# Kernel tuning notes

Hardware: AMD Instinct MI355X
Metric: run time of the kernel (lower is better)

The kernel has to match this reference:

```python
import jax, jax.numpy as jnp
import numpy as np

EMBED = 512
KDIM = 512
VDIM = 512
HEADS = 8
DHEAD = EMBED // HEADS  # 64
SCALE = 1.0 / np.sqrt(DHEAD).astype(np.float32)


def setup_inputs() -> dict:
    key = jax.random.key(0)
    ks = jax.random.split(key, 11)
    B, Lq, Lk = 4, 2048, 2048
    s_in = 1.0 / np.sqrt(EMBED).astype(np.float32)
    return {
        "query": jax.random.normal(ks[0], (B, Lq, EMBED), jnp.float32),
        "key": jax.random.normal(ks[1], (B, Lk, KDIM), jnp.float32),
        "value": jax.random.normal(ks[2], (B, Lk, VDIM), jnp.float32),
        "wq": jax.random.normal(ks[3], (EMBED, KDIM), jnp.float32) * s_in,
        "bq": jnp.zeros((KDIM,), jnp.float32),
        "wk": jax.random.normal(ks[4], (KDIM, KDIM), jnp.float32) * s_in,
        "bk": jnp.zeros((KDIM,), jnp.float32),
        "wv": jax.random.normal(ks[5], (VDIM, VDIM), jnp.float32) * s_in,
        "bv": jnp.zeros((VDIM,), jnp.float32),
        "wo": jax.random.normal(ks[6], (VDIM, EMBED), jnp.float32) * s_in,
        "bo": jnp.zeros((EMBED,), jnp.float32),
    }


def _split_heads(x):
    b, l, _ = x.shape
    return x.reshape(b, l, HEADS, DHEAD).transpose(0, 2, 1, 3)  # b h l d


def reference(query, key, value, wq, bq, wk, bk, wv, bv, wo, bo):
    # Linear projections (weights stored [in, out])
    q = _split_heads(query @ wq + bq)   # b h Lq d
    k = _split_heads(key @ wk + bk)     # b h Lk d
    v = _split_heads(value @ wv + bv)   # b h Lk d
    scores = jnp.einsum('bhid,bhjd->bhij', q, k) * SCALE  # b h Lq Lk
    attn = jax.nn.softmax(scores, axis=-1)
    # dropout is identity in eval mode
    ctx = jnp.einsum('bhij,bhjd->bhid', attn, v)  # b h Lq d
    b, h, l, d = ctx.shape
    ctx = ctx.transpose(0, 2, 1, 3).reshape(b, l, h * d)  # b Lq vdim
    return ctx @ wo + bo
```

## Files before the change

kernel.cpp:

```cpp
#include <hip/hip_runtime.h>
#include <stdint.h>

typedef unsigned short u16;
typedef unsigned int u32;
typedef __attribute__((ext_vector_type(8))) short short8;
typedef __attribute__((ext_vector_type(4))) float f32x4;
typedef __attribute__((ext_vector_type(16))) float f32x16;

#define DEVI static __device__ __forceinline__

DEVI u16 f2bf(float f) {
  union { float f; u32 u; } v; v.f = f;
  u32 r = v.u + 0x7FFFu + ((v.u >> 16) & 1u);
  return (u16)(r >> 16);
}

DEVI u32 pack2bf(float lo, float hi) {
  return (u32)f2bf(lo) | ((u32)f2bf(hi) << 16);
}

DEVI u32 pack2bf_fast(float lo, float hi) {
  union { float f; u32 u; } a, b;
  a.f = lo; b.f = hi;
  return __builtin_amdgcn_perm(b.u + 0x8000u, a.u + 0x8000u, 0x07060302u);
}

DEVI void gload_lds16(const u16* g, u16* l) {
  __builtin_amdgcn_global_load_lds((const __attribute__((address_space(1))) void*)g,
                                   (__attribute__((address_space(3))) void*)l, 16, 0, 0);
}

__global__ __launch_bounds__(256) void cvt3(const float* __restrict__ s0,
                                            const float* __restrict__ s1,
                                            const float* __restrict__ s2,
                                            u16* __restrict__ d0, u16* __restrict__ d1,
                                            u16* __restrict__ d2, int n) {
  int z = blockIdx.z;
  const float* src = z == 0 ? s0 : z == 1 ? s1 : s2;
  u16* dst = z == 0 ? d0 : z == 1 ? d1 : d2;
  int i = (blockIdx.x * 256 + threadIdx.x) * 4;
  if (i >= n) return;
  float4 v = *(const float4*)(src + i);
  uint2 o;
  o.x = pack2bf(v.x, v.y);
  o.y = pack2bf(v.z, v.w);
  *(uint2*)(dst + i) = o;
}

__global__ __launch_bounds__(256) void tw4(const float* __restrict__ s0, const float* __restrict__ s1,
                                           const float* __restrict__ s2, const float* __restrict__ s3,
                                           u16* __restrict__ d0, u16* __restrict__ d1,
                                           u16* __restrict__ d2, u16* __restrict__ d3) {
  int z = blockIdx.z;
  const float* src = z == 0 ? s0 : z == 1 ? s1 : z == 2 ? s2 : s3;
  u16* dst = z == 0 ? d0 : z == 1 ? d1 : z == 2 ? d2 : d3;
  __shared__ float tile[32][33];
  int tx = threadIdx.x & 31, ty = threadIdx.x >> 5;
  int bx = blockIdx.x * 32, by = blockIdx.y * 32;
#pragma unroll
  for (int i = 0; i < 32; i += 8)
    tile[ty + i][tx] = src[(size_t)(by + ty + i) * 512 + bx + tx];
  __syncthreads();
#pragma unroll
  for (int i = 0; i < 32; i += 8)
    dst[(size_t)(bx + ty + i) * 512 + by + tx] = f2bf(tile[tx][ty + i]);
}

__global__ __launch_bounds__(256) void gemm_qkv(
    const u16* __restrict__ A0, const u16* __restrict__ A1, const u16* __restrict__ A2,
    const u16* __restrict__ W0, const u16* __restrict__ W1, const u16* __restrict__ W2,
    const float* __restrict__ b0, const float* __restrict__ b1, const float* __restrict__ b2,
    u16* __restrict__ o0, u16* __restrict__ o1, u16* __restrict__ o2, float qscale) {
  const int z = blockIdx.z;
  const u16* A = z == 0 ? A0 : z == 1 ? A1 : A2;
  const u16* WT = z == 0 ? W0 : z == 1 ? W1 : W2;
  const float* bias = z == 0 ? b0 : z == 1 ? b1 : b2;
  u16* out = z == 0 ? o0 : z == 1 ? o1 : o2;
  const float sc = z == 0 ? qscale : 1.0f;

  __shared__ __align__(16) u16 As[128 * 64];
  __shared__ __align__(16) u16 Bs[128 * 64];
  const int t = threadIdx.x;
  const int w = t >> 6, lane = t & 63, quad = lane >> 4, li = lane & 15;
  const int m0 = blockIdx.x * 128, n0 = blockIdx.y * 128;
  const int wm = (w >> 1) * 64, wn = (w & 1) * 64;

  f32x4 zv = {0.f, 0.f, 0.f, 0.f};
  f32x4 acc[4][4];
#pragma unroll
  for (int mi = 0; mi < 4; mi++)
#pragma unroll
    for (int ni = 0; ni < 4; ni++) acc[mi][ni] = zv;

  for (int it = 0; it < 8; it++) {
    const int k0 = it * 64;
#pragma unroll
    for (int i = 0; i < 4; i++) {
      int s = i * 256 + t;
      int r = s >> 3, c8 = s & 7;
      gload_lds16(A + (size_t)(m0 + r) * 512 + k0 + ((c8 ^ (r & 7)) * 8),
                  &As[(i * 256 + w * 64) * 8]);
    }
#pragma unroll
    for (int i = 0; i < 4; i++) {
      int s = i * 256 + t;
      int r = s >> 3, c8 = s & 7;
      gload_lds16(WT + (size_t)(n0 + r) * 512 + k0 + ((c8 ^ (r & 7)) * 8),
                  &Bs[(i * 256 + w * 64) * 8]);
    }
    __syncthreads();
#pragma unroll
    for (int ks = 0; ks < 2; ks++) {
      short8 af[4], bf[4];
#pragma unroll
      for (int mi = 0; mi < 4; mi++) {
        int r = wm + mi * 16 + li;
        af[mi] = *(const short8*)&As[r * 64 + (((ks * 4 + quad) ^ (r & 7)) * 8)];
      }
#pragma unroll
      for (int ni = 0; ni < 4; ni++) {
        int r = wn + ni * 16 + li;
        bf[ni] = *(const short8*)&Bs[r * 64 + (((ks * 4 + quad) ^ (r & 7)) * 8)];
      }
#pragma unroll
      for (int mi = 0; mi < 4; mi++)
#pragma unroll
        for (int ni = 0; ni < 4; ni++)
          acc[mi][ni] = __builtin_amdgcn_mfma_f32_16x16x32_bf16(af[mi], bf[ni], acc[mi][ni], 0, 0, 0);
    }
    __syncthreads();
  }

  float bv[4];
#pragma unroll
  for (int ni = 0; ni < 4; ni++) bv[ni] = bias[n0 + wn + ni * 16 + li];
#pragma unroll
  for (int mi = 0; mi < 4; mi++)
#pragma unroll
    for (int ni = 0; ni < 4; ni++)
#pragma unroll
      for (int r = 0; r < 4; r++) {
        int row = m0 + wm + mi * 16 + quad * 4 + r;
        int col = n0 + wn + ni * 16 + li;
        out[(size_t)row * 512 + col] = f2bf((acc[mi][ni][r] + bv[ni]) * sc);
      }
}

__global__ __launch_bounds__(256) void gemm_out(const u16* __restrict__ A,
                                                const u16* __restrict__ WT,
                                                const float* __restrict__ bias,
                                                float* __restrict__ out) {
  __shared__ __align__(16) u16 As[128 * 64];
  __shared__ __align__(16) u16 Bs[64 * 64];
  const int t = threadIdx.x;
  const int w = t >> 6, lane = t & 63, quad = lane >> 4, li = lane & 15;
  const int m0 = blockIdx.x * 128, n0 = blockIdx.y * 64;
  const int wm = (w >> 1) * 64, wn = (w & 1) * 32;

  f32x4 zv = {0.f, 0.f, 0.f, 0.f};
  f32x4 acc[4][2];
#pragma unroll
  for (int mi = 0; mi < 4; mi++)
#pragma unroll
    for (int ni = 0; ni < 2; ni++) acc[mi][ni] = zv;

  for (int it = 0; it < 8; it++) {
    const int k0 = it * 64;
#pragma unroll
    for (int i = 0; i < 4; i++) {
      int s = i * 256 + t;
      int r = s >> 3, c8 = s & 7;
      gload_lds16(A + (size_t)(m0 + r) * 512 + k0 + ((c8 ^ (r & 7)) * 8),
                  &As[(i * 256 + w * 64) * 8]);
    }
#pragma unroll
    for (int i = 0; i < 2; i++) {
      int s = i * 256 + t;
      int r = s >> 3, c8 = s & 7;
      gload_lds16(WT + (size_t)(n0 + r) * 512 + k0 + ((c8 ^ (r & 7)) * 8),
                  &Bs[(i * 256 + w * 64) * 8]);
    }
    __syncthreads();
#pragma unroll
    for (int ks = 0; ks < 2; ks++) {
      short8 af[4], bf[2];
#pragma unroll
      for (int mi = 0; mi < 4; mi++) {
        int r = wm + mi * 16 + li;
        af[mi] = *(const short8*)&As[r * 64 + (((ks * 4 + quad) ^ (r & 7)) * 8)];
      }
#pragma unroll
      for (int ni = 0; ni < 2; ni++) {
        int r = wn + ni * 16 + li;
        bf[ni] = *(const short8*)&Bs[r * 64 + (((ks * 4 + quad) ^ (r & 7)) * 8)];
      }
#pragma unroll
      for (int mi = 0; mi < 4; mi++)
#pragma unroll
        for (int ni = 0; ni < 2; ni++)
          acc[mi][ni] = __builtin_amdgcn_mfma_f32_16x16x32_bf16(af[mi], bf[ni], acc[mi][ni], 0, 0, 0);
    }
    __syncthreads();
  }

  float bv[2];
#pragma unroll
  for (int ni = 0; ni < 2; ni++) bv[ni] = bias[n0 + wn + ni * 16 + li];
#pragma unroll
  for (int mi = 0; mi < 4; mi++)
#pragma unroll
    for (int ni = 0; ni < 2; ni++)
#pragma unroll
      for (int r = 0; r < 4; r++) {
        int row = m0 + wm + mi * 16 + quad * 4 + r;
        int col = n0 + wn + ni * 16 + li;
        out[(size_t)row * 512 + col] = acc[mi][ni][r] + bv[ni];
      }
}

__global__ __launch_bounds__(256) void transpose_v(const u16* __restrict__ Vp,
                                                   u16* __restrict__ VT) {
  __shared__ u16 tile[64][65];
  int b = blockIdx.z, h = blockIdx.y, l0 = blockIdx.x * 64;
  int t = threadIdx.x;
#pragma unroll
  for (int p = 0; p < 2; p++) {
    int r = (t >> 3) + p * 32, c = (t & 7) * 8;
    short8 v = *(const short8*)&Vp[(size_t)(b * 2048 + l0 + r) * 512 + h * 64 + c];
#pragma unroll
    for (int i = 0; i < 8; i++) tile[r][c + i] = (u16)v[i];
  }
  __syncthreads();
  int d = t >> 2, lc = (t & 3) * 16;
  u16* o = VT + ((size_t)((b * 8 + h) * 64 + d)) * 2048 + l0 + lc;
  short8 o0, o1;
#pragma unroll
  for (int i = 0; i < 8; i++) o0[i] = (short)tile[lc + i][d];
#pragma unroll
  for (int i = 0; i < 8; i++) o1[i] = (short)tile[lc + 8 + i][d];
  *(short8*)(o) = o0;
  *(short8*)(o + 8) = o1;
}

__global__ __launch_bounds__(256) void attn(const u16* __restrict__ Qp,
                                            const u16* __restrict__ Kp,
                                            const u16* __restrict__ VT,
                                            u16* __restrict__ ctx) {
  __shared__ __align__(16) u16 Ks[64 * 64];
  __shared__ __align__(16) u16 Vs[64 * 64];
  __shared__ __align__(16) u16 Ps[4][32 * 64];
  const int t = threadIdx.x;
  const int w = t >> 6, lane = t & 63;
  const int qn = lane & 31, hi = lane >> 5;
  const int b = blockIdx.z, h = blockIdx.y;
  const int q0 = blockIdx.x * 128 + w * 32;

  short8 qf[4];
  {
    const u16* qg = Qp + (size_t)(b * 2048 + q0 + qn) * 512 + h * 64 + hi * 8;
#pragma unroll
    for (int ks = 0; ks < 4; ks++) qf[ks] = *(const short8*)(qg + ks * 16);
  }

  f32x16 o[2];
#pragma unroll
  for (int dt = 0; dt < 2; dt++)
#pragma unroll
    for (int r = 0; r < 16; r++) o[dt][r] = 0.f;
  float lsum = 0.f;

  u16* pw = &Ps[w][0];

  for (int kt = 0; kt < 32; kt++) {
    const int k0 = kt * 64;
#pragma unroll
    for (int i = 0; i < 2; i++) {
      int s = i * 256 + t;
      int r = s >> 3, c8 = s & 7;
      gload_lds16(Kp + (size_t)(b * 2048 + k0 + r) * 512 + h * 64 + ((c8 ^ (r & 7)) * 8),
                  &Ks[(i * 256 + w * 64) * 8]);
      gload_lds16(VT + ((size_t)((b * 8 + h) * 64 + r)) * 2048 + k0 + ((c8 ^ (r & 7)) * 8),
                  &Vs[(i * 256 + w * 64) * 8]);
    }
    __syncthreads();

    f32x16 st[2];
#pragma unroll
    for (int kjt = 0; kjt < 2; kjt++) {
#pragma unroll
      for (int r = 0; r < 16; r++) st[kjt][r] = 0.f;
#pragma unroll
      for (int ks = 0; ks < 4; ks++) {
        int m = kjt * 32 + qn;
        short8 ka = *(const short8*)&Ks[m * 64 + (((ks * 2 + hi) ^ (m & 7)) * 8)];
        st[kjt] = __builtin_amdgcn_mfma_f32_32x32x16_bf16(ka, qf[ks], st[kjt], 0, 0, 0);
      }
    }

#pragma unroll
    for (int kjt = 0; kjt < 2; kjt++)
#pragma unroll
      for (int k8 = 0; k8 < 4; k8++) {
        float p0 = __builtin_amdgcn_exp2f(st[kjt][k8 * 4 + 0]);
        float p1 = __builtin_amdgcn_exp2f(st[kjt][k8 * 4 + 1]);
        float p2 = __builtin_amdgcn_exp2f(st[kjt][k8 * 4 + 2]);
        float p3 = __builtin_amdgcn_exp2f(st[kjt][k8 * 4 + 3]);
        lsum += (p0 + p1) + (p2 + p3);
        uint2 dw;
        dw.x = pack2bf_fast(p0, p1);
        dw.y = pack2bf_fast(p2, p3);
        int chunk = kjt * 4 + k8;
        *(uint2*)&pw[qn * 64 + ((chunk ^ (qn & 7)) * 8) + hi * 4] = dw;
      }

    short8 pb[4];
#pragma unroll
    for (int ks = 0; ks < 4; ks++)
      pb[ks] = *(const short8*)&pw[qn * 64 + (((ks * 2 + hi) ^ (qn & 7)) * 8)];
#pragma unroll
    for (int dt = 0; dt < 2; dt++)
#pragma unroll
      for (int ks = 0; ks < 4; ks++) {
        int m = dt * 32 + qn;
        short8 va = *(const short8*)&Vs[m * 64 + (((ks * 2 + hi) ^ (m & 7)) * 8)];
        o[dt] = __builtin_amdgcn_mfma_f32_32x32x16_bf16(va, pb[ks], o[dt], 0, 0, 0);
      }
    __syncthreads();
  }

  float l = lsum + __shfl_xor(lsum, 32);
  float inv = 1.0f / l;

#pragma unroll
  for (int dt = 0; dt < 2; dt++)
#pragma unroll
    for (int k8 = 0; k8 < 4; k8++) {
      uint2 dw;
      dw.x = pack2bf_fast(o[dt][k8 * 4 + 0] * inv, o[dt][k8 * 4 + 1] * inv);
      dw.y = pack2bf_fast(o[dt][k8 * 4 + 2] * inv, o[dt][k8 * 4 + 3] * inv);
      int chunk = dt * 4 + k8;
      *(uint2*)&pw[qn * 64 + ((chunk ^ (qn & 7)) * 8) + hi * 4] = dw;
    }
  __builtin_amdgcn_s_waitcnt(0);
  int q = lane >> 1, half = lane & 1;
  u16* dst = ctx + (size_t)(b * 2048 + q0 + q) * 512 + h * 64 + half * 32;
#pragma unroll
  for (int cc = 0; cc < 4; cc++) {
    int chunk = half * 4 + cc;
    *(short8*)(dst + cc * 8) = *(const short8*)&pw[q * 64 + ((chunk ^ (q & 7)) * 8)];
  }
}

extern "C" void kernel_launch(void* const* d_in, const int* in_sizes, int n_in,
                              void* d_out, int out_size, void* d_ws, size_t ws_size,
                              hipStream_t stream) {
  const float* query = (const float*)d_in[0];
  const float* key_ = (const float*)d_in[1];
  const float* value = (const float*)d_in[2];
  const float* wq = (const float*)d_in[3];
  const float* bq = (const float*)d_in[4];
  const float* wk = (const float*)d_in[5];
  const float* bk = (const float*)d_in[6];
  const float* wv = (const float*)d_in[7];
  const float* bv = (const float*)d_in[8];
  const float* wo = (const float*)d_in[9];
  const float* bo = (const float*)d_in[10];

  char* ws = (char*)d_ws;
  const size_t SZ_X = (size_t)8192 * 512 * 2;
  const size_t SZ_W = (size_t)512 * 512 * 2;
  u16* qb = (u16*)(ws);
  u16* kb = (u16*)(ws + SZ_X);
  u16* vb = (u16*)(ws + 2 * SZ_X);
  u16* wqT = (u16*)(ws + 3 * SZ_X);
  u16* wkT = (u16*)(ws + 3 * SZ_X + SZ_W);
  u16* wvT = (u16*)(ws + 3 * SZ_X + 2 * SZ_W);
  u16* woT = (u16*)(ws + 3 * SZ_X + 3 * SZ_W);
  u16* Qp = (u16*)(ws + 3 * SZ_X + 4 * SZ_W);
  u16* Kp = (u16*)(ws + 4 * SZ_X + 4 * SZ_W);
  u16* Vp = (u16*)(ws + 5 * SZ_X + 4 * SZ_W);
  u16* VTp = kb;
  u16* ctx = qb;

  const float C1 = 0.125f * 1.44269504088896f;

  const int n = 8192 * 512;
  cvt3<<<dim3(n / 1024, 1, 3), 256, 0, stream>>>(query, key_, value, qb, kb, vb, n);
  tw4<<<dim3(16, 16, 4), 256, 0, stream>>>(wq, wk, wv, wo, wqT, wkT, wvT, woT);
  gemm_qkv<<<dim3(64, 4, 3), 256, 0, stream>>>(qb, kb, vb, wqT, wkT, wvT, bq, bk, bv,
                                               Qp, Kp, Vp, C1);
  transpose_v<<<dim3(32, 8, 4), 256, 0, stream>>>(Vp, VTp);
  attn<<<dim3(16, 8, 4), 256, 0, stream>>>(Qp, Kp, VTp, ctx);
  gemm_out<<<dim3(64, 8), 256, 0, stream>>>(ctx, woT, bo, (float*)d_out);
}
```

Before: 207.1 us.

## Fuse input conversion and V transpose into QKV GEMM, split attention over keys

Removes the separate fp32-to-bf16 conversion kernel by converting the inputs inside the QKV GEMM load path. The V-transpose kernel is also dropped: the V projection now writes its output already transposed. Attention now splits the key range in two across blocks, with 128-thread blocks each handling 128 queries. This gives a split-K partial output plus row sums, merged and normalized by a new reduce kernel. The output GEMM uses a wider N tile, and the LDS swizzle gains an extra XOR term. The cost is fp32 partial-output traffic and one extra reduction launch, in exchange for fewer launches and more attention parallelism.

```diff
diff --git a/kernel.cpp b/kernel.cpp
--- a/kernel.cpp
+++ b/kernel.cpp
@@ -30,22 +30,7 @@
                                    (__attribute__((address_space(3))) void*)l, 16, 0, 0);
 }
 
-__global__ __launch_bounds__(256) void cvt3(const float* __restrict__ s0,
-                                            const float* __restrict__ s1,
-                                            const float* __restrict__ s2,
-                                            u16* __restrict__ d0, u16* __restrict__ d1,
-                                            u16* __restrict__ d2, int n) {
-  int z = blockIdx.z;
-  const float* src = z == 0 ? s0 : z == 1 ? s1 : s2;
-  u16* dst = z == 0 ? d0 : z == 1 ? d1 : d2;
-  int i = (blockIdx.x * 256 + threadIdx.x) * 4;
-  if (i >= n) return;
-  float4 v = *(const float4*)(src + i);
-  uint2 o;
-  o.x = pack2bf(v.x, v.y);
-  o.y = pack2bf(v.z, v.w);
-  *(uint2*)(dst + i) = o;
-}
+DEVI int sw8(int chunk, int r) { return ((chunk ^ (r & 7) ^ ((r >> 3) & 3)) * 8); }
 
 __global__ __launch_bounds__(256) void tw4(const float* __restrict__ s0, const float* __restrict__ s1,
                                            const float* __restrict__ s2, const float* __restrict__ s3,
@@ -67,15 +52,14 @@
 }
 
 __global__ __launch_bounds__(256) void gemm_qkv(
-    const u16* __restrict__ A0, const u16* __restrict__ A1, const u16* __restrict__ A2,
+    const float* __restrict__ A0, const float* __restrict__ A1, const float* __restrict__ A2,
     const u16* __restrict__ W0, const u16* __restrict__ W1, const u16* __restrict__ W2,
     const float* __restrict__ b0, const float* __restrict__ b1, const float* __restrict__ b2,
-    u16* __restrict__ o0, u16* __restrict__ o1, u16* __restrict__ o2, float qscale) {
+    u16* __restrict__ oq, u16* __restrict__ ok, u16* __restrict__ vt, float qscale) {
   const int z = blockIdx.z;
-  const u16* A = z == 0 ? A0 : z == 1 ? A1 : A2;
+  const float* A = z == 0 ? A0 : z == 1 ? A1 : A2;
   const u16* WT = z == 0 ? W0 : z == 1 ? W1 : W2;
   const float* bias = z == 0 ? b0 : z == 1 ? b1 : b2;
-  u16* out = z == 0 ? o0 : z == 1 ? o1 : o2;
   const float sc = z == 0 ? qscale : 1.0f;
 
   __shared__ __align__(16) u16 As[128 * 64];
@@ -92,21 +76,27 @@
 #pragma unroll
     for (int ni = 0; ni < 4; ni++) acc[mi][ni] = zv;
 
+  const int rA = t >> 3, cA = t & 7;
   for (int it = 0; it < 8; it++) {
     const int k0 = it * 64;
 #pragma unroll
-    for (int i = 0; i < 4; i++) {
-      int s = i * 256 + t;
+    for (int p = 0; p < 4; p++) {
+      int r = p * 32 + rA;
+      const float* ga = A + (size_t)(m0 + r) * 512 + k0 + cA * 8;
+      float4 f0 = *(const float4*)ga;
+      float4 f1 = *(const float4*)(ga + 4);
+      uint4 pk;
+      pk.x = pack2bf_fast(f0.x, f0.y);
+      pk.y = pack2bf_fast(f0.z, f0.w);
+      pk.z = pack2bf_fast(f1.x, f1.y);
+      pk.w = pack2bf_fast(f1.z, f1.w);
+      *(uint4*)&As[r * 64 + sw8(cA, r)] = pk;
+    }
+#pragma unroll
+    for (int p = 0; p < 4; p++) {
+      int s = p * 256 + t;
       int r = s >> 3, c8 = s & 7;
-      gload_lds16(A + (size_t)(m0 + r) * 512 + k0 + ((c8 ^ (r & 7)) * 8),
-                  &As[(i * 256 + w * 64) * 8]);
-    }
-#pragma unroll
-    for (int i = 0; i < 4; i++) {
-      int s = i * 256 + t;
-      int r = s >> 3, c8 = s & 7;
-      gload_lds16(WT + (size_t)(n0 + r) * 512 + k0 + ((c8 ^ (r & 7)) * 8),
-                  &Bs[(i * 256 + w * 64) * 8]);
+      gload_lds16(WT + (size_t)(n0 + r) * 512 + k0 + sw8(c8, r), &Bs[(p * 256 + w * 64) * 8]);
     }
     __syncthreads();
 #pragma unroll
@@ -115,12 +105,12 @@
 #pragma unroll
       for (int mi = 0; mi < 4; mi++) {
         int r = wm + mi * 16 + li;
-        af[mi] = *(const short8*)&As[r * 64 + (((ks * 4 + quad) ^ (r & 7)) * 8)];
+        af[mi] = *(const short8*)&As[r * 64 + sw8(ks * 4 + quad, r)];
       }
 #pragma unroll
       for (int ni = 0; ni < 4; ni++) {
         int r = wn + ni * 16 + li;
-        bf[ni] = *(const short8*)&Bs[r * 64 + (((ks * 4 + quad) ^ (r & 7)) * 8)];
+        bf[ni] = *(const short8*)&Bs[r * 64 + sw8(ks * 4 + quad, r)];
       }
 #pragma unroll
       for (int mi = 0; mi < 4; mi++)
@@ -134,16 +124,34 @@
   float bv[4];
 #pragma unroll
   for (int ni = 0; ni < 4; ni++) bv[ni] = bias[n0 + wn + ni * 16 + li];
-#pragma unroll
-  for (int mi = 0; mi < 4; mi++)
-#pragma unroll
-    for (int ni = 0; ni < 4; ni++)
-#pragma unroll
-      for (int r = 0; r < 4; r++) {
-        int row = m0 + wm + mi * 16 + quad * 4 + r;
+
+  if (z < 2) {
+    u16* out = z == 0 ? oq : ok;
+#pragma unroll
+    for (int mi = 0; mi < 4; mi++)
+#pragma unroll
+      for (int ni = 0; ni < 4; ni++)
+#pragma unroll
+        for (int r = 0; r < 4; r++) {
+          int row = m0 + wm + mi * 16 + quad * 4 + r;
+          int col = n0 + wn + ni * 16 + li;
+          out[(size_t)row * 512 + col] = f2bf((acc[mi][ni][r] + bv[ni]) * sc);
+        }
+  } else {
+#pragma unroll
+    for (int mi = 0; mi < 4; mi++)
+#pragma unroll
+      for (int ni = 0; ni < 4; ni++) {
         int col = n0 + wn + ni * 16 + li;
-        out[(size_t)row * 512 + col] = f2bf((acc[mi][ni][r] + bv[ni]) * sc);
-      }
+        int h = col >> 6, dd = col & 63;
+        int row0 = m0 + wm + mi * 16 + quad * 4;
+        int bb = row0 >> 11, l0 = row0 & 2047;
+        uint2 dw;
+        dw.x = pack2bf(acc[mi][ni][0] + bv[ni], acc[mi][ni][1] + bv[ni]);
+        dw.y = pack2bf(acc[mi][ni][2] + bv[ni], acc[mi][ni][3] + bv[ni]);
+        *(uint2*)&vt[((size_t)((bb * 8 + h) * 64 + dd)) * 2048 + l0] = dw;
+      }
+  }
 }
 
 __global__ __launch_bounds__(256) void gemm_out(const u16* __restrict__ A,
@@ -151,65 +159,58 @@
                                                 const float* __restrict__ bias,
                                                 float* __restrict__ out) {
   __shared__ __align__(16) u16 As[128 * 64];
-  __shared__ __align__(16) u16 Bs[64 * 64];
+  __shared__ __align__(16) u16 Bs[128 * 64];
   const int t = threadIdx.x;
   const int w = t >> 6, lane = t & 63, quad = lane >> 4, li = lane & 15;
-  const int m0 = blockIdx.x * 128, n0 = blockIdx.y * 64;
-  const int wm = (w >> 1) * 64, wn = (w & 1) * 32;
+  const int m0 = blockIdx.x * 128, n0 = blockIdx.y * 128;
+  const int wm = (w >> 1) * 64, wn = (w & 1) * 64;
 
   f32x4 zv = {0.f, 0.f, 0.f, 0.f};
-  f32x4 acc[4][2];
+  f32x4 acc[4][4];
 #pragma unroll
   for (int mi = 0; mi < 4; mi++)
 #pragma unroll
-    for (int ni = 0; ni < 2; ni++) acc[mi][ni] = zv;
+    for (int ni = 0; ni < 4; ni++) acc[mi][ni] = zv;
 
   for (int it = 0; it < 8; it++) {
     const int k0 = it * 64;
 #pragma unroll
-    for (int i = 0; i < 4; i++) {
-      int s = i * 256 + t;
+    for (int p = 0; p < 4; p++) {
+      int s = p * 256 + t;
       int r = s >> 3, c8 = s & 7;
-      gload_lds16(A + (size_t)(m0 + r) * 512 + k0 + ((c8 ^ (r & 7)) * 8),
-                  &As[(i * 256 + w * 64) * 8]);
-    }
-#pragma unroll
-    for (int i = 0; i < 2; i++) {
-      int s = i * 256 + t;
-      int r = s >> 3, c8 = s & 7;
-      gload_lds16(WT + (size_t)(n0 + r) * 512 + k0 + ((c8 ^ (r & 7)) * 8),
-                  &Bs[(i * 256 + w * 64) * 8]);
+      gload_lds16(A + (size_t)(m0 + r) * 512 + k0 + sw8(c8, r), &As[(p * 256 + w * 64) * 8]);
+      gload_lds16(WT + (size_t)(n0 + r) * 512 + k0 + sw8(c8, r), &Bs[(p * 256 + w * 64) * 8]);
     }
     __syncthreads();
 #pragma unroll
     for (int ks = 0; ks < 2; ks++) {
-      short8 af[4], bf[2];
+      short8 af[4], bf[4];
 #pragma unroll
       for (int mi = 0; mi < 4; mi++) {
         int r = wm + mi * 16 + li;
-        af[mi] = *(const short8*)&As[r * 64 + (((ks * 4 + quad) ^ (r & 7)) * 8)];
-      }
-#pragma unroll
-      for (int ni = 0; ni < 2; ni++) {
+        af[mi] = *(const short8*)&As[r * 64 + sw8(ks * 4 + quad, r)];
+      }
+#pragma unroll
+      for (int ni = 0; ni < 4; ni++) {
         int r = wn + ni * 16 + li;
-        bf[ni] = *(const short8*)&Bs[r * 64 + (((ks * 4 + quad) ^ (r & 7)) * 8)];
+        bf[ni] = *(const short8*)&Bs[r * 64 + sw8(ks * 4 + quad, r)];
       }
 #pragma unroll
       for (int mi = 0; mi < 4; mi++)
 #pragma unroll
-        for (int ni = 0; ni < 2; ni++)
+        for (int ni = 0; ni < 4; ni++)
           acc[mi][ni] = __builtin_amdgcn_mfma_f32_16x16x32_bf16(af[mi], bf[ni], acc[mi][ni], 0, 0, 0);
     }
     __syncthreads();
   }
 
-  float bv[2];
-#pragma unroll
-  for (int ni = 0; ni < 2; ni++) bv[ni] = bias[n0 + wn + ni * 16 + li];
+  float bv[4];
+#pragma unroll
+  for (int ni = 0; ni < 4; ni++) bv[ni] = bias[n0 + wn + ni * 16 + li];
 #pragma unroll
   for (int mi = 0; mi < 4; mi++)
 #pragma unroll
-    for (int ni = 0; ni < 2; ni++)
+    for (int ni = 0; ni < 4; ni++)
 #pragma unroll
       for (int r = 0; r < 4; r++) {
         int row = m0 + wm + mi * 16 + quad * 4 + r;
@@ -218,136 +219,156 @@
       }
 }
 
-__global__ __launch_bounds__(256) void transpose_v(const u16* __restrict__ Vp,
-                                                   u16* __restrict__ VT) {
-  __shared__ u16 tile[64][65];
-  int b = blockIdx.z, h = blockIdx.y, l0 = blockIdx.x * 64;
-  int t = threadIdx.x;
-#pragma unroll
-  for (int p = 0; p < 2; p++) {
-    int r = (t >> 3) + p * 32, c = (t & 7) * 8;
-    short8 v = *(const short8*)&Vp[(size_t)(b * 2048 + l0 + r) * 512 + h * 64 + c];
-#pragma unroll
-    for (int i = 0; i < 8; i++) tile[r][c + i] = (u16)v[i];
-  }
-  __syncthreads();
-  int d = t >> 2, lc = (t & 3) * 16;
-  u16* o = VT + ((size_t)((b * 8 + h) * 64 + d)) * 2048 + l0 + lc;
-  short8 o0, o1;
-#pragma unroll
-  for (int i = 0; i < 8; i++) o0[i] = (short)tile[lc + i][d];
-#pragma unroll
-  for (int i = 0; i < 8; i++) o1[i] = (short)tile[lc + 8 + i][d];
-  *(short8*)(o) = o0;
-  *(short8*)(o + 8) = o1;
-}
-
-__global__ __launch_bounds__(256) void attn(const u16* __restrict__ Qp,
+__global__ __launch_bounds__(128) void attn(const u16* __restrict__ Qp,
                                             const u16* __restrict__ Kp,
                                             const u16* __restrict__ VT,
-                                            u16* __restrict__ ctx) {
+                                            float* __restrict__ Op,
+                                            float* __restrict__ Lb) {
   __shared__ __align__(16) u16 Ks[64 * 64];
   __shared__ __align__(16) u16 Vs[64 * 64];
   __shared__ __align__(16) u16 Ps[4][32 * 64];
   const int t = threadIdx.x;
-  const int w = t >> 6, lane = t & 63;
-  const int qn = lane & 31, hi = lane >> 5;
-  const int b = blockIdx.z, h = blockIdx.y;
-  const int q0 = blockIdx.x * 128 + w * 32;
-
-  short8 qf[4];
+  const int w = t >> 6, lane = t & 63, qn = lane & 31, hi = lane >> 5;
+  const int b = blockIdx.z, h = blockIdx.y >> 1, s = blockIdx.y & 1;
+  const int q0 = blockIdx.x * 128;
+
+  u16* Qs = &Ps[0][0];
+#pragma unroll
+  for (int i = 0; i < 8; i++) {
+    int si = i * 128 + t;
+    int r = si >> 3, c8 = si & 7;
+    gload_lds16(Qp + (size_t)(b * 2048 + q0 + r) * 512 + h * 64 + sw8(c8, r),
+                &Qs[(i * 128 + w * 64) * 8]);
+  }
+  __syncthreads();
+  short8 qf[2][4];
+#pragma unroll
+  for (int u = 0; u < 2; u++)
+#pragma unroll
+    for (int ks = 0; ks < 4; ks++) {
+      int rq = w * 64 + u * 32 + qn;
+      qf[u][ks] = *(const short8*)&Qs[rq * 64 + sw8(ks * 2 + hi, rq)];
+    }
+
+  f32x16 o[2][2];
+#pragma unroll
+  for (int u = 0; u < 2; u++)
+#pragma unroll
+    for (int dt = 0; dt < 2; dt++)
+#pragma unroll
+      for (int r = 0; r < 16; r++) o[u][dt][r] = 0.f;
+  float lsum[2] = {0.f, 0.f};
+
+  for (int kt = s * 16; kt < s * 16 + 16; kt++) {
+    const int k0 = kt * 64;
+#pragma unroll
+    for (int i = 0; i < 4; i++) {
+      int si = i * 128 + t;
+      int r = si >> 3, c8 = si & 7;
+      gload_lds16(Kp + (size_t)(b * 2048 + k0 + r) * 512 + h * 64 + sw8(c8, r),
+                  &Ks[(i * 128 + w * 64) * 8]);
+      gload_lds16(VT + ((size_t)((b * 8 + h) * 64 + r)) * 2048 + k0 + sw8(c8, r),
+                  &Vs[(i * 128 + w * 64) * 8]);
+    }
+    __syncthreads();
+
+#pragma unroll
+    for (int u = 0; u < 2; u++) {
+      f32x16 st[2];
+#pragma unroll
+      for (int kjt = 0; kjt < 2; kjt++) {
+#pragma unroll
+        for (int r = 0; r < 16; r++) st[kjt][r] = 0.f;
+#pragma unroll
+        for (int ks = 0; ks < 4; ks++) {
+          int m = kjt * 32 + qn;
+          short8 ka = *(const short8*)&Ks[m * 64 + sw8(ks * 2 + hi, m)];
+          st[kjt] = __builtin_amdgcn_mfma_f32_32x32x16_bf16(ka, qf[u][ks], st[kjt], 0, 0, 0);
+        }
+      }
+
+      u16* pw = &Ps[w * 2 + u][0];
+#pragma unroll
+      for (int kjt = 0; kjt < 2; kjt++)
+#pragma unroll
+        for (int k8 = 0; k8 < 4; k8++) {
+          float p0 = __builtin_amdgcn_exp2f(st[kjt][k8 * 4 + 0]);
+          float p1 = __builtin_amdgcn_exp2f(st[kjt][k8 * 4 + 1]);
+          float p2 = __builtin_amdgcn_exp2f(st[kjt][k8 * 4 + 2]);
+          float p3 = __builtin_amdgcn_exp2f(st[kjt][k8 * 4 + 3]);
+          lsum[u] += (p0 + p1) + (p2 + p3);
+          uint2 dw;
+          dw.x = pack2bf_fast(p0, p1);
+          dw.y = pack2bf_fast(p2, p3);
+          *(uint2*)&pw[qn * 64 + sw8(kjt * 4 + k8, qn) + hi * 4] = dw;
+        }
+
+      short8 pb[4];
+#pragma unroll
+      for (int ks = 0; ks < 4; ks++)
+        pb[ks] = *(const short8*)&pw[qn * 64 + sw8(ks * 2 + hi, qn)];
+#pragma unroll
+      for (int dt = 0; dt < 2; dt++)
+#pragma unroll
+        for (int ks = 0; ks < 4; ks++) {
+          int m = dt * 32 + qn;
+          short8 va = *(const short8*)&Vs[m * 64 + sw8(ks * 2 + hi, m)];
+          o[u][dt] = __builtin_amdgcn_mfma_f32_32x32x16_bf16(va, pb[ks], o[u][dt], 0, 0, 0);
+        }
+    }
+    __syncthreads();
+  }
+
+#pragma unroll
+  for (int u = 0; u < 2; u++) {
+    float l = lsum[u] + __shfl_xor(lsum[u], 32);
+    int qg = q0 + w * 64 + u * 32 + qn;
+    if (hi == 0) Lb[((size_t)((b * 8 + h) * 2 + s)) * 2048 + qg] = l;
+#pragma unroll
+    for (int dt = 0; dt < 2; dt++)
+#pragma unroll
+      for (int r = 0; r < 16; r++) {
+        int d = dt * 32 + (r & 3) + 8 * (r >> 2) + 4 * hi;
+        Op[((size_t)(((b * 8 + h) * 2 + s) * 64 + d)) * 2048 + qg] = o[u][dt][r];
+      }
+  }
+}
+
+__global__ __launch_bounds__(256) void reduce_o(const float* __restrict__ Op,
+                                                const float* __restrict__ Lb,
+                                                u16* __restrict__ ctx) {
+  __shared__ float tile[64 * 65];
+  const int t = threadIdx.x;
+  const int b = blockIdx.z, h = blockIdx.y, q0 = blockIdx.x * 64;
   {
-    const u16* qg = Qp + (size_t)(b * 2048 + q0 + qn) * 512 + h * 64 + hi * 8;
-#pragma unroll
-    for (int ks = 0; ks < 4; ks++) qf[ks] = *(const short8*)(qg + ks * 16);
-  }
-
-  f32x16 o[2];
-#pragma unroll
-  for (int dt = 0; dt < 2; dt++)
-#pragma unroll
-    for (int r = 0; r < 16; r++) o[dt][r] = 0.f;
-  float lsum = 0.f;
-
-  u16* pw = &Ps[w][0];
-
-  for (int kt = 0; kt < 32; kt++) {
-    const int k0 = kt * 64;
-#pragma unroll
-    for (int i = 0; i < 2; i++) {
-      int s = i * 256 + t;
-      int r = s >> 3, c8 = s & 7;
-      gload_lds16(Kp + (size_t)(b * 2048 + k0 + r) * 512 + h * 64 + ((c8 ^ (r & 7)) * 8),
-                  &Ks[(i * 256 + w * 64) * 8]);
-      gload_lds16(VT + ((size_t)((b * 8 + h) * 64 + r)) * 2048 + k0 + ((c8 ^ (r & 7)) * 8),
-                  &Vs[(i * 256 + w * 64) * 8]);
-    }
-    __syncthreads();
-
-    f32x16 st[2];
-#pragma unroll
-    for (int kjt = 0; kjt < 2; kjt++) {
-#pragma unroll
-      for (int r = 0; r < 16; r++) st[kjt][r] = 0.f;
-#pragma unroll
-      for (int ks = 0; ks < 4; ks++) {
-        int m = kjt * 32 + qn;
-        short8 ka = *(const short8*)&Ks[m * 64 + (((ks * 2 + hi) ^ (m & 7)) * 8)];
-        st[kjt] = __builtin_amdgcn_mfma_f32_32x32x16_bf16(ka, qf[ks], st[kjt], 0, 0, 0);
-      }
-    }
-
-#pragma unroll
-    for (int kjt = 0; kjt < 2; kjt++)
-#pragma unroll
-      for (int k8 = 0; k8 < 4; k8++) {
-        float p0 = __builtin_amdgcn_exp2f(st[kjt][k8 * 4 + 0]);
-        float p1 = __builtin_amdgcn_exp2f(st[kjt][k8 * 4 + 1]);
-        float p2 = __builtin_amdgcn_exp2f(st[kjt][k8 * 4 + 2]);
-        float p3 = __builtin_amdgcn_exp2f(st[kjt][k8 * 4 + 3]);
-        lsum += (p0 + p1) + (p2 + p3);
-        uint2 dw;
-        dw.x = pack2bf_fast(p0, p1);
-        dw.y = pack2bf_fast(p2, p3);
-        int chunk = kjt * 4 + k8;
-        *(uint2*)&pw[qn * 64 + ((chunk ^ (qn & 7)) * 8) + hi * 4] = dw;
-      }
-
-    short8 pb[4];
-#pragma unroll
-    for (int ks = 0; ks < 4; ks++)
-      pb[ks] = *(const short8*)&pw[qn * 64 + (((ks * 2 + hi) ^ (qn & 7)) * 8)];
-#pragma unroll
-    for (int dt = 0; dt < 2; dt++)
-#pragma unroll
-      for (int ks = 0; ks < 4; ks++) {
-        int m = dt * 32 + qn;
-        short8 va = *(const short8*)&Vs[m * 64 + (((ks * 2 + hi) ^ (m & 7)) * 8)];
-        o[dt] = __builtin_amdgcn_mfma_f32_32x32x16_bf16(va, pb[ks], o[dt], 0, 0, 0);
-      }
-    __syncthreads();
-  }
-
-  float l = lsum + __shfl_xor(lsum, 32);
-  float inv = 1.0f / l;
-
-#pragma unroll
-  for (int dt = 0; dt < 2; dt++)
-#pragma unroll
-    for (int k8 = 0; k8 < 4; k8++) {
-      uint2 dw;
-      dw.x = pack2bf_fast(o[dt][k8 * 4 + 0] * inv, o[dt][k8 * 4 + 1] * inv);
-      dw.y = pack2bf_fast(o[dt][k8 * 4 + 2] * inv, o[dt][k8 * 4 + 3] * inv);
-      int chunk = dt * 4 + k8;
-      *(uint2*)&pw[qn * 64 + ((chunk ^ (qn & 7)) * 8) + hi * 4] = dw;
-    }
-  __builtin_amdgcn_s_waitcnt(0);
-  int q = lane >> 1, half = lane & 1;
-  u16* dst = ctx + (size_t)(b * 2048 + q0 + q) * 512 + h * 64 + half * 32;
-#pragma unroll
-  for (int cc = 0; cc < 4; cc++) {
-    int chunk = half * 4 + cc;
-    *(short8*)(dst + cc * 8) = *(const short8*)&pw[q * 64 + ((chunk ^ (q & 7)) * 8)];
+    int d = t >> 2, qc = (t & 3) * 16;
+    const float* p0 = Op + ((size_t)(((b * 8 + h) * 2 + 0) * 64 + d)) * 2048 + q0 + qc;
+    const float* p1 = Op + ((size_t)(((b * 8 + h) * 2 + 1) * 64 + d)) * 2048 + q0 + qc;
+#pragma unroll
+    for (int i = 0; i < 4; i++) {
+      float4 a = *(const float4*)(p0 + i * 4);
+      float4 c = *(const float4*)(p1 + i * 4);
+      float4 v;
+      v.x = a.x + c.x; v.y = a.y + c.y; v.z = a.z + c.z; v.w = a.w + c.w;
+      *(float4*)&tile[d * 65 + qc + i * 4] = v;
+    }
+  }
+  __syncthreads();
+  {
+    int q = t >> 2, dc = (t & 3) * 16;
+    float l0 = Lb[((size_t)((b * 8 + h) * 2 + 0)) * 2048 + q0 + q];
+    float l1 = Lb[((size_t)((b * 8 + h) * 2 + 1)) * 2048 + q0 + q];
+    float inv = 1.0f / (l0 + l1);
+    u32 pk[8];
+#pragma unroll
+    for (int i = 0; i < 8; i++) {
+      float v0 = tile[(dc + i * 2) * 65 + q] * inv;
+      float v1 = tile[(dc + i * 2 + 1) * 65 + q] * inv;
+      pk[i] = pack2bf(v0, v1);
+    }
+    u16* dst = ctx + (size_t)(b * 2048 + q0 + q) * 512 + h * 64 + dc;
+    *(uint4*)dst = *(uint4*)&pk[0];
+    *(uint4*)(dst + 8) = *(uint4*)&pk[4];
   }
 }
 
@@ -367,29 +388,25 @@
   const float* bo = (const float*)d_in[10];
 
   char* ws = (char*)d_ws;
+  const size_t SZ_W = (size_t)512 * 512 * 2;
   const size_t SZ_X = (size_t)8192 * 512 * 2;
-  const size_t SZ_W = (size_t)512 * 512 * 2;
-  u16* qb = (u16*)(ws);
-  u16* kb = (u16*)(ws + SZ_X);
-  u16* vb = (u16*)(ws + 2 * SZ_X);
-  u16* wqT = (u16*)(ws + 3 * SZ_X);
-  u16* wkT = (u16*)(ws + 3 * SZ_X + SZ_W);
-  u16* wvT = (u16*)(ws + 3 * SZ_X + 2 * SZ_W);
-  u16* woT = (u16*)(ws + 3 * SZ_X + 3 * SZ_W);
-  u16* Qp = (u16*)(ws + 3 * SZ_X + 4 * SZ_W);
-  u16* Kp = (u16*)(ws + 4 * SZ_X + 4 * SZ_W);
-  u16* Vp = (u16*)(ws + 5 * SZ_X + 4 * SZ_W);
-  u16* VTp = kb;
-  u16* ctx = qb;
+  u16* wqT = (u16*)(ws);
+  u16* wkT = (u16*)(ws + SZ_W);
+  u16* wvT = (u16*)(ws + 2 * SZ_W);
+  u16* woT = (u16*)(ws + 3 * SZ_W);
+  u16* Qp = (u16*)(ws + 4 * SZ_W);
+  u16* Kp = (u16*)(ws + 4 * SZ_W + SZ_X);
+  u16* VTp = (u16*)(ws + 4 * SZ_W + 2 * SZ_X);
+  float* Opb = (float*)(ws + 4 * SZ_W + 3 * SZ_X);
+  float* Lb = (float*)(ws + 4 * SZ_W + 3 * SZ_X + ((size_t)32 << 20));
+  u16* ctx = Qp;
 
   const float C1 = 0.125f * 1.44269504088896f;
 
-  const int n = 8192 * 512;
-  cvt3<<<dim3(n / 1024, 1, 3), 256, 0, stream>>>(query, key_, value, qb, kb, vb, n);
   tw4<<<dim3(16, 16, 4), 256, 0, stream>>>(wq, wk, wv, wo, wqT, wkT, wvT, woT);
-  gemm_qkv<<<dim3(64, 4, 3), 256, 0, stream>>>(qb, kb, vb, wqT, wkT, wvT, bq, bk, bv,
-                                               Qp, Kp, Vp, C1);
-  transpose_v<<<dim3(32, 8, 4), 256, 0, stream>>>(Vp, VTp);
-  attn<<<dim3(16, 8, 4), 256, 0, stream>>>(Qp, Kp, VTp, ctx);
-  gemm_out<<<dim3(64, 8), 256, 0, stream>>>(ctx, woT, bo, (float*)d_out);
-}
+  gemm_qkv<<<dim3(64, 4, 3), 256, 0, stream>>>(query, key_, value, wqT, wkT, wvT,
+                                               bq, bk, bv, Qp, Kp, VTp, C1);
+  attn<<<dim3(16, 16, 4), 128, 0, stream>>>(Qp, Kp, VTp, Opb, Lb);
+  reduce_o<<<dim3(32, 8, 4), 256, 0, stream>>>(Opb, Lb, ctx);
+  gemm_out<<<dim3(64, 4), 256, 0, stream>>>(ctx, woT, bo, (float*)d_out);
+}
```

After: 210.4 us. No clear change (+1.6%).
